# Optimization experiments

Hardware: AMD Instinct MI355X
Metric: run time of the kernel (lower is better)

Reference implementation:

```python
import jax, jax.numpy as jnp
import numpy as np

N_NODES = 50000

def setup_inputs() -> dict:
    key = jax.random.key(0)
    k1, k2, k3, k4, k5, k6, k7 = jax.random.split(key, 7)
    d_in, d_hid, d_out = 128, 512, 128
    n_edges = 600000
    x = jax.random.normal(k1, (N_NODES, d_in), dtype=jnp.float32)
    edge_index = jax.random.randint(k2, (2, n_edges), 0, N_NODES, dtype=jnp.int64)
    edge_weight = jax.random.uniform(k3, (n_edges,), dtype=jnp.float32)
    # GCNConv params (PyG: weight [in, out], bias [out])
    W1 = jax.random.normal(k4, (d_in, d_hid), dtype=jnp.float32) / np.sqrt(d_in)
    b1 = jax.random.normal(k5, (d_hid,), dtype=jnp.float32) * 0.01
    W2 = jax.random.normal(k6, (d_hid, d_out), dtype=jnp.float32) / np.sqrt(d_hid)
    b2 = jax.random.normal(k7, (d_out,), dtype=jnp.float32) * 0.01
    return {"x": x, "edge_index": edge_index, "edge_weight": edge_weight,
            "W1": W1, "b1": b1, "W2": W2, "b2": b2}

def gcn_conv(x, src, dst, ew, W, b, n_nodes):
    # PyG GCNConv: add self-loops (weight 1), symmetric normalization
    idx = jnp.arange(n_nodes, dtype=src.dtype)
    src_f = jnp.concatenate([src, idx])
    dst_f = jnp.concatenate([dst, idx])
    ew_f = jnp.concatenate([ew, jnp.ones((n_nodes,), dtype=ew.dtype)])
    deg = jax.ops.segment_sum(ew_f, dst_f, num_segments=n_nodes)
    dinv = jnp.where(deg > 0, jax.lax.rsqrt(deg), 0.0)
    norm = dinv[src_f] * ew_f * dinv[dst_f]  # [E+N]
    xw = x @ W  # [N, d_hid]
    msg = xw[src_f] * norm[:, None]  # [E+N, d_hid]
    agg = jax.ops.segment_sum(msg, dst_f, num_segments=n_nodes)
    return agg + b

def reference(x, edge_index, edge_weight, W1, b1, W2, b2):
    src, dst = edge_index[0], edge_index[1]
    h = gcn_conv(x, src, dst, edge_weight, W1, b1, N_NODES)
    h = jax.nn.relu(h)
    out = jax.nn.relu(h @ W2 + b2)
    return out
```

## Files before the change

### kernel.cpp

```cpp
#include <hip/hip_runtime.h>
#include <math.h>


typedef __attribute__((ext_vector_type(8))) short short8v;
typedef __attribute__((ext_vector_type(4))) float floatx4;

__device__ __forceinline__ short f2bf(float f) {
    unsigned u = __builtin_bit_cast(unsigned, f);
    unsigned r = (u + 0x7FFFu + ((u >> 16) & 1u)) >> 16;
    return (short)r;
}
__device__ __forceinline__ float bf2f(short s) {
    return __builtin_bit_cast(float, ((unsigned)(unsigned short)s) << 16);
}


__global__ __launch_bounds__(256) void k_init(int* __restrict__ counts,
                                              float* __restrict__ deg, int n) {
    int i = blockIdx.x * 256 + threadIdx.x;
    if (i < n) { counts[i] = 0; deg[i] = 1.0f; }
}

__global__ __launch_bounds__(256) void k_hist(const int* __restrict__ dst,
                                              const float* __restrict__ ew,
                                              int* __restrict__ counts,
                                              float* __restrict__ deg, int E) {
    int e = blockIdx.x * 256 + threadIdx.x;
    if (e < E) {
        int d = dst[e];
        atomicAdd(&counts[d], 1);
        atomicAdd(&deg[d], ew[e]);
    }
}

__global__ __launch_bounds__(256) void k_scanA(const int* __restrict__ counts,
                                               int* __restrict__ offsets,
                                               int* __restrict__ blockSum,
                                               float* __restrict__ deg, int n) {
    __shared__ int sdata[256];
    const int tid = threadIdx.x;
    const int i = blockIdx.x * 256 + tid;
    int c = (i < n) ? counts[i] : 0;
    sdata[tid] = c;
    __syncthreads();
#pragma unroll
    for (int off = 1; off < 256; off <<= 1) {
        int t = (tid >= off) ? sdata[tid - off] : 0;
        __syncthreads();
        sdata[tid] += t;
        __syncthreads();
    }
    if (i < n) offsets[i] = sdata[tid] - c;
    if (tid == 255) blockSum[blockIdx.x] = sdata[255];
    if (i < n) {
        float d = deg[i];
        deg[i] = (d > 0.f) ? rsqrtf(d) : 0.f;
    }
}

__global__ __launch_bounds__(256) void k_scanB(int* __restrict__ blockSum, int nb) {
    __shared__ int sdata[256];
    const int tid = threadIdx.x;
    int v = (tid < nb) ? blockSum[tid] : 0;
    sdata[tid] = v;
    __syncthreads();
#pragma unroll
    for (int off = 1; off < 256; off <<= 1) {
        int t = (tid >= off) ? sdata[tid - off] : 0;
        __syncthreads();
        sdata[tid] += t;
        __syncthreads();
    }
    if (tid < nb) blockSum[tid] = sdata[tid] - v;
}

__global__ __launch_bounds__(256) void k_scanC(int* __restrict__ offsets,
                                               const int* __restrict__ blockSum,
                                               int* __restrict__ cursor, int n, int E) {
    const int i = blockIdx.x * 256 + threadIdx.x;
    if (i < n) {
        int o = offsets[i] + blockSum[blockIdx.x];
        offsets[i] = o;
        cursor[i] = o;
    }
    if (i == 0) offsets[n] = E;
}

__global__ __launch_bounds__(256) void k_scatter(const int* __restrict__ src,
                                                 const int* __restrict__ dst,
                                                 const float* __restrict__ ew,
                                                 const float* __restrict__ dinv,
                                                 int* __restrict__ cursor,
                                                 int2* __restrict__ sedge, int E) {
    int e = blockIdx.x * 256 + threadIdx.x;
    if (e >= E) return;
    int s = src[e];
    int d = dst[e];
    float coef = dinv[s] * ew[e] * dinv[d];
    int pos = atomicAdd(&cursor[d], 1);
    sedge[pos] = make_int2(s, __builtin_bit_cast(int, coef));
}

__global__ __launch_bounds__(256) void k_gather(const int* __restrict__ offsets,
                                                const int2* __restrict__ sedge,
                                                const float* __restrict__ dinv,
                                                const float* __restrict__ x,
                                                float* __restrict__ y, int n) {
    int wid = (blockIdx.x * 256 + threadIdx.x) >> 6;
    if (wid >= n) return;
    int lane = threadIdx.x & 63;
    int o0 = offsets[wid];
    int o1 = offsets[wid + 1];
    float di = dinv[wid];
    const float2* x2 = (const float2*)x;
    float2 xv = x2[(size_t)wid * 64 + lane];
    float2 acc;
    acc.x = di * di * xv.x;
    acc.y = di * di * xv.y;
    int j = o0;
    for (; j + 4 <= o1; j += 4) {
        int2 e0 = sedge[j], e1 = sedge[j + 1], e2 = sedge[j + 2], e3 = sedge[j + 3];
        float2 v0 = x2[(size_t)e0.x * 64 + lane];
        float2 v1 = x2[(size_t)e1.x * 64 + lane];
        float2 v2 = x2[(size_t)e2.x * 64 + lane];
        float2 v3 = x2[(size_t)e3.x * 64 + lane];
        float c0 = __builtin_bit_cast(float, e0.y);
        float c1 = __builtin_bit_cast(float, e1.y);
        float c2 = __builtin_bit_cast(float, e2.y);
        float c3 = __builtin_bit_cast(float, e3.y);
        acc.x = fmaf(c0, v0.x, acc.x); acc.y = fmaf(c0, v0.y, acc.y);
        acc.x = fmaf(c1, v1.x, acc.x); acc.y = fmaf(c1, v1.y, acc.y);
        acc.x = fmaf(c2, v2.x, acc.x); acc.y = fmaf(c2, v2.y, acc.y);
        acc.x = fmaf(c3, v3.x, acc.x); acc.y = fmaf(c3, v3.y, acc.y);
    }
    for (; j < o1; ++j) {
        int2 e = sedge[j];
        float2 v = x2[(size_t)e.x * 64 + lane];
        float c = __builtin_bit_cast(float, e.y);
        acc.x = fmaf(c, v.x, acc.x);
        acc.y = fmaf(c, v.y, acc.y);
    }
    ((float2*)y)[(size_t)wid * 64 + lane] = acc;
}

__global__ __launch_bounds__(256) void k_wprep(const float* __restrict__ W1,
                                               const float* __restrict__ W2,
                                               short* __restrict__ W1t,
                                               short* __restrict__ W2t) {
    int i = blockIdx.x * 256 + threadIdx.x;
    if (i < 65536) {
        int c = i >> 7, k = i & 127;
        W1t[i] = f2bf(W1[k * 512 + c]);
    } else if (i < 131072) {
        int j = i - 65536;
        int c = j >> 9, k = j & 511;
        W2t[j] = f2bf(W2[k * 128 + c]);
    }
}

__global__ __launch_bounds__(256) void k_mlp(const float* __restrict__ y,
                                             const short* __restrict__ W1t,
                                             const float* __restrict__ b1,
                                             const short* __restrict__ W2t,
                                             const float* __restrict__ b2,
                                             float* __restrict__ out, int n) {
    __shared__ __align__(16) short hlds[32 * 512];
    const int tid  = threadIdx.x;
    const int wave = tid >> 6;
    const int lane = tid & 63;
    const int l15  = lane & 15;
    const int lg   = lane >> 4;
    const int row0 = blockIdx.x * 32;

    const int cb1 = wave * 128;
    floatx4 acc[2][8];
#pragma unroll
    for (int m = 0; m < 2; ++m)
#pragma unroll
        for (int nn = 0; nn < 8; ++nn) acc[m][nn] = (floatx4)0.0f;

#pragma unroll
    for (int kk = 0; kk < 4; ++kk) {
        const int k0 = kk * 32 + lg * 8;
        short8v bf[8];
#pragma unroll
        for (int nn = 0; nn < 8; ++nn)
            bf[nn] = *(const short8v*)(W1t + (size_t)(cb1 + nn * 16 + l15) * 128 + k0);
#pragma unroll
        for (int m = 0; m < 2; ++m) {
            const float* ap = y + (size_t)(row0 + m * 16 + l15) * 128 + k0;
            float4 f0 = *(const float4*)ap;
            float4 f1 = *(const float4*)(ap + 4);
            float fv[8] = {f0.x, f0.y, f0.z, f0.w, f1.x, f1.y, f1.z, f1.w};
            short8v ahi, alo;
#pragma unroll
            for (int i = 0; i < 8; ++i) {
                short h = f2bf(fv[i]);
                ahi[i] = h;
                alo[i] = f2bf(fv[i] - bf2f(h));
            }
#pragma unroll
            for (int nn = 0; nn < 8; ++nn)
                acc[m][nn] = __builtin_amdgcn_mfma_f32_16x16x32_bf16(ahi, bf[nn], acc[m][nn], 0, 0, 0);
#pragma unroll
            for (int nn = 0; nn < 8; ++nn)
                acc[m][nn] = __builtin_amdgcn_mfma_f32_16x16x32_bf16(alo, bf[nn], acc[m][nn], 0, 0, 0);
        }
    }

#pragma unroll
    for (int m = 0; m < 2; ++m)
#pragma unroll
        for (int nn = 0; nn < 8; ++nn) {
            const int c = cb1 + nn * 16 + l15;
            const float bb = b1[c];
#pragma unroll
            for (int i = 0; i < 4; ++i) {
                const int r = m * 16 + lg * 4 + i;
                float v = acc[m][nn][i] + bb;
                v = v > 0.f ? v : 0.f;
                hlds[r * 512 + (c ^ ((r & 7) << 3))] = f2bf(v);
            }
        }
    __syncthreads();

    const int cb2 = wave * 32;
    floatx4 acc2[2][2];
#pragma unroll
    for (int m = 0; m < 2; ++m)
#pragma unroll
        for (int nn = 0; nn < 2; ++nn) acc2[m][nn] = (floatx4)0.0f;

#pragma unroll
    for (int kk = 0; kk < 16; ++kk) {
        const int k0 = kk * 32 + lg * 8;
        short8v bf2[2];
#pragma unroll
        for (int nn = 0; nn < 2; ++nn)
            bf2[nn] = *(const short8v*)(W2t + (size_t)(cb2 + nn * 16 + l15) * 512 + k0);
#pragma unroll
        for (int m = 0; m < 2; ++m) {
            const int r = m * 16 + l15;
            short8v a = *(const short8v*)&hlds[r * 512 + (k0 ^ ((r & 7) << 3))];
#pragma unroll
            for (int nn = 0; nn < 2; ++nn)
                acc2[m][nn] = __builtin_amdgcn_mfma_f32_16x16x32_bf16(a, bf2[nn], acc2[m][nn], 0, 0, 0);
        }
    }

#pragma unroll
    for (int m = 0; m < 2; ++m)
#pragma unroll
        for (int nn = 0; nn < 2; ++nn) {
            const int c = cb2 + nn * 16 + l15;
            const float bb = b2[c];
#pragma unroll
            for (int i = 0; i < 4; ++i) {
                const int rg = row0 + m * 16 + lg * 4 + i;
                if (rg < n) {
                    float v = acc2[m][nn][i] + bb;
                    out[(size_t)rg * 128 + c] = v > 0.f ? v : 0.f;
                }
            }
        }
}

extern "C" void kernel_launch(void* const* d_in, const int* in_sizes, int n_in,
                              void* d_out, int out_size, void* d_ws, size_t ws_size,
                              hipStream_t stream) {
    const float* x  = (const float*)d_in[0];
    const int*   ei = (const int*)d_in[1];
    const float* ew = (const float*)d_in[2];
    const float* W1 = (const float*)d_in[3];
    const float* b1 = (const float*)d_in[4];
    const float* W2 = (const float*)d_in[5];
    const float* b2 = (const float*)d_in[6];
    float* out = (float*)d_out;

    const int N = in_sizes[0] / 128;
    const int E = in_sizes[2];
    const int* src = ei;
    const int* dst = ei + E;
    const int NB = (N + 255) / 256;

    float* y        = (float*)d_ws;
    float* deg      = y + (size_t)N * 128;
    int*   counts   = (int*)(deg + N);
    int*   offsets  = counts + N;
    int*   cursor   = offsets + N + 1;
    int*   blockSum = cursor + N;
    int2*  sedge    = (int2*)((((uintptr_t)(blockSum + 256)) + 15) & ~(uintptr_t)15);
    short* W1t      = (short*)(sedge + E);
    short* W2t      = W1t + 65536;

    int nb;
    k_wprep<<<512, 256, 0, stream>>>(W1, W2, W1t, W2t);
    nb = (N + 255) / 256;
    k_init<<<nb, 256, 0, stream>>>(counts, deg, N);
    nb = (E + 255) / 256;
    k_hist<<<nb, 256, 0, stream>>>(dst, ew, counts, deg, E);
    k_scanA<<<NB, 256, 0, stream>>>(counts, offsets, blockSum, deg, N);
    k_scanB<<<1, 256, 0, stream>>>(blockSum, NB);
    k_scanC<<<NB, 256, 0, stream>>>(offsets, blockSum, cursor, N, E);
    nb = (E + 255) / 256;
    k_scatter<<<nb, 256, 0, stream>>>(src, dst, ew, deg, cursor, sedge, E);
    nb = (N * 64 + 255) / 256;
    k_gather<<<nb, 256, 0, stream>>>(offsets, sedge, deg, x, y, N);
    nb = (N + 31) / 32;
    k_mlp<<<nb, 256, 0, stream>>>(y, W1t, b1, W2t, b2, out, N);
}
```

Before: 303.9 us.

## Fuse neighbor gather into MLP kernel via swizzled LDS, merge init with weight prep

The gather stage now runs inside the MLP kernel. Each block aggregates its 32 node rows into LDS as bf16 hi/lo pairs with an XOR swizzle, which removes the N×128 fp32 intermediate written to and read back from global memory. The separate cursor array is dropped: scatter advances offsets in place, and gather recovers each start as end minus count. The init and weight-prep kernels are merged to save a launch, but each MLP block now does gather work with only 4 waves of 8 rows, so there is less latency hiding for the random gathers.

```diff
diff --git a/kernel.cpp b/kernel.cpp
--- a/kernel.cpp
+++ b/kernel.cpp
@@ -14,11 +14,22 @@
     return __builtin_bit_cast(float, ((unsigned)(unsigned short)s) << 16);
 }
 
-
-__global__ __launch_bounds__(256) void k_init(int* __restrict__ counts,
-                                              float* __restrict__ deg, int n) {
+__global__ __launch_bounds__(256) void k_initprep(int* __restrict__ counts,
+                                                  float* __restrict__ deg, int n,
+                                                  const float* __restrict__ W1,
+                                                  const float* __restrict__ W2,
+                                                  short* __restrict__ W1t,
+                                                  short* __restrict__ W2t) {
     int i = blockIdx.x * 256 + threadIdx.x;
     if (i < n) { counts[i] = 0; deg[i] = 1.0f; }
+    if (i < 65536) {
+        int c = i >> 7, k = i & 127;
+        W1t[i] = f2bf(W1[k * 512 + c]);
+    } else if (i < 131072) {
+        int j = i - 65536;
+        int c = j >> 9, k = j & 511;
+        W2t[j] = f2bf(W2[k * 128 + c]);
+    }
 }
 
 __global__ __launch_bounds__(256) void k_hist(const int* __restrict__ dst,
@@ -75,95 +86,38 @@
 }
 
 __global__ __launch_bounds__(256) void k_scanC(int* __restrict__ offsets,
-                                               const int* __restrict__ blockSum,
-                                               int* __restrict__ cursor, int n, int E) {
+                                               const int* __restrict__ blockSum, int n) {
     const int i = blockIdx.x * 256 + threadIdx.x;
-    if (i < n) {
-        int o = offsets[i] + blockSum[blockIdx.x];
-        offsets[i] = o;
-        cursor[i] = o;
-    }
-    if (i == 0) offsets[n] = E;
+    if (i < n) offsets[i] += blockSum[blockIdx.x];
 }
 
 __global__ __launch_bounds__(256) void k_scatter(const int* __restrict__ src,
                                                  const int* __restrict__ dst,
                                                  const float* __restrict__ ew,
                                                  const float* __restrict__ dinv,
-                                                 int* __restrict__ cursor,
+                                                 int* __restrict__ offsets,
                                                  int2* __restrict__ sedge, int E) {
     int e = blockIdx.x * 256 + threadIdx.x;
     if (e >= E) return;
     int s = src[e];
     int d = dst[e];
     float coef = dinv[s] * ew[e] * dinv[d];
-    int pos = atomicAdd(&cursor[d], 1);
+    int pos = atomicAdd(&offsets[d], 1);
     sedge[pos] = make_int2(s, __builtin_bit_cast(int, coef));
 }
 
-__global__ __launch_bounds__(256) void k_gather(const int* __restrict__ offsets,
-                                                const int2* __restrict__ sedge,
-                                                const float* __restrict__ dinv,
-                                                const float* __restrict__ x,
-                                                float* __restrict__ y, int n) {
-    int wid = (blockIdx.x * 256 + threadIdx.x) >> 6;
-    if (wid >= n) return;
-    int lane = threadIdx.x & 63;
-    int o0 = offsets[wid];
-    int o1 = offsets[wid + 1];
-    float di = dinv[wid];
-    const float2* x2 = (const float2*)x;
-    float2 xv = x2[(size_t)wid * 64 + lane];
-    float2 acc;
-    acc.x = di * di * xv.x;
-    acc.y = di * di * xv.y;
-    int j = o0;
-    for (; j + 4 <= o1; j += 4) {
-        int2 e0 = sedge[j], e1 = sedge[j + 1], e2 = sedge[j + 2], e3 = sedge[j + 3];
-        float2 v0 = x2[(size_t)e0.x * 64 + lane];
-        float2 v1 = x2[(size_t)e1.x * 64 + lane];
-        float2 v2 = x2[(size_t)e2.x * 64 + lane];
-        float2 v3 = x2[(size_t)e3.x * 64 + lane];
-        float c0 = __builtin_bit_cast(float, e0.y);
-        float c1 = __builtin_bit_cast(float, e1.y);
-        float c2 = __builtin_bit_cast(float, e2.y);
-        float c3 = __builtin_bit_cast(float, e3.y);
-        acc.x = fmaf(c0, v0.x, acc.x); acc.y = fmaf(c0, v0.y, acc.y);
-        acc.x = fmaf(c1, v1.x, acc.x); acc.y = fmaf(c1, v1.y, acc.y);
-        acc.x = fmaf(c2, v2.x, acc.x); acc.y = fmaf(c2, v2.y, acc.y);
-        acc.x = fmaf(c3, v3.x, acc.x); acc.y = fmaf(c3, v3.y, acc.y);
-    }
-    for (; j < o1; ++j) {
-        int2 e = sedge[j];
-        float2 v = x2[(size_t)e.x * 64 + lane];
-        float c = __builtin_bit_cast(float, e.y);
-        acc.x = fmaf(c, v.x, acc.x);
-        acc.y = fmaf(c, v.y, acc.y);
-    }
-    ((float2*)y)[(size_t)wid * 64 + lane] = acc;
-}
-
-__global__ __launch_bounds__(256) void k_wprep(const float* __restrict__ W1,
-                                               const float* __restrict__ W2,
-                                               short* __restrict__ W1t,
-                                               short* __restrict__ W2t) {
-    int i = blockIdx.x * 256 + threadIdx.x;
-    if (i < 65536) {
-        int c = i >> 7, k = i & 127;
-        W1t[i] = f2bf(W1[k * 512 + c]);
-    } else if (i < 131072) {
-        int j = i - 65536;
-        int c = j >> 9, k = j & 511;
-        W2t[j] = f2bf(W2[k * 128 + c]);
-    }
-}
-
-__global__ __launch_bounds__(256) void k_mlp(const float* __restrict__ y,
-                                             const short* __restrict__ W1t,
-                                             const float* __restrict__ b1,
-                                             const short* __restrict__ W2t,
-                                             const float* __restrict__ b2,
-                                             float* __restrict__ out, int n) {
+__global__ __launch_bounds__(256) void k_gmlp(const int* __restrict__ offsets,
+                                              const int* __restrict__ counts,
+                                              const int2* __restrict__ sedge,
+                                              const float* __restrict__ dinv,
+                                              const float* __restrict__ x,
+                                              const short* __restrict__ W1t,
+                                              const float* __restrict__ b1,
+                                              const short* __restrict__ W2t,
+                                              const float* __restrict__ b2,
+                                              float* __restrict__ out, int n) {
+    __shared__ __align__(16) short yhi[32 * 128];
+    __shared__ __align__(16) short ylo[32 * 128];
     __shared__ __align__(16) short hlds[32 * 512];
     const int tid  = threadIdx.x;
     const int wave = tid >> 6;
@@ -171,6 +125,52 @@
     const int l15  = lane & 15;
     const int lg   = lane >> 4;
     const int row0 = blockIdx.x * 32;
+    const float2* x2 = (const float2*)x;
+
+    for (int i = 0; i < 8; ++i) {
+        const int r = wave * 8 + i;
+        const int node = row0 + r;
+        float2 acc = make_float2(0.f, 0.f);
+        if (node < n) {
+            int o1 = offsets[node];
+            int o0 = o1 - counts[node];
+            float di = dinv[node];
+            float2 xv = x2[(size_t)node * 64 + lane];
+            acc.x = di * di * xv.x;
+            acc.y = di * di * xv.y;
+            int j = o0;
+            for (; j + 4 <= o1; j += 4) {
+                int2 e0 = sedge[j], e1 = sedge[j + 1], e2 = sedge[j + 2], e3 = sedge[j + 3];
+                float2 v0 = x2[(size_t)e0.x * 64 + lane];
+                float2 v1 = x2[(size_t)e1.x * 64 + lane];
+                float2 v2 = x2[(size_t)e2.x * 64 + lane];
+                float2 v3 = x2[(size_t)e3.x * 64 + lane];
+                float c0 = __builtin_bit_cast(float, e0.y);
+                float c1 = __builtin_bit_cast(float, e1.y);
+                float c2 = __builtin_bit_cast(float, e2.y);
+                float c3 = __builtin_bit_cast(float, e3.y);
+                acc.x = fmaf(c0, v0.x, acc.x); acc.y = fmaf(c0, v0.y, acc.y);
+                acc.x = fmaf(c1, v1.x, acc.x); acc.y = fmaf(c1, v1.y, acc.y);
+                acc.x = fmaf(c2, v2.x, acc.x); acc.y = fmaf(c2, v2.y, acc.y);
+                acc.x = fmaf(c3, v3.x, acc.x); acc.y = fmaf(c3, v3.y, acc.y);
+            }
+            for (; j < o1; ++j) {
+                int2 e = sedge[j];
+                float2 v = x2[(size_t)e.x * 64 + lane];
+                float c = __builtin_bit_cast(float, e.y);
+                acc.x = fmaf(c, v.x, acc.x);
+                acc.y = fmaf(c, v.y, acc.y);
+            }
+        }
+        short hx = f2bf(acc.x);
+        short hy = f2bf(acc.y);
+        short lx = f2bf(acc.x - bf2f(hx));
+        short ly = f2bf(acc.y - bf2f(hy));
+        const int e = (2 * lane) ^ ((r & 7) << 3);
+        *(short2*)&yhi[r * 128 + e] = make_short2(hx, hy);
+        *(short2*)&ylo[r * 128 + e] = make_short2(lx, ly);
+    }
+    __syncthreads();
 
     const int cb1 = wave * 128;
     floatx4 acc[2][8];
@@ -188,17 +188,10 @@
             bf[nn] = *(const short8v*)(W1t + (size_t)(cb1 + nn * 16 + l15) * 128 + k0);
 #pragma unroll
         for (int m = 0; m < 2; ++m) {
-            const float* ap = y + (size_t)(row0 + m * 16 + l15) * 128 + k0;
-            float4 f0 = *(const float4*)ap;
-            float4 f1 = *(const float4*)(ap + 4);
-            float fv[8] = {f0.x, f0.y, f0.z, f0.w, f1.x, f1.y, f1.z, f1.w};
-            short8v ahi, alo;
-#pragma unroll
-            for (int i = 0; i < 8; ++i) {
-                short h = f2bf(fv[i]);
-                ahi[i] = h;
-                alo[i] = f2bf(fv[i] - bf2f(h));
-            }
+            const int r = m * 16 + l15;
+            const int ke = k0 ^ ((r & 7) << 3);
+            short8v ahi = *(const short8v*)&yhi[r * 128 + ke];
+            short8v alo = *(const short8v*)&ylo[r * 128 + ke];
 #pragma unroll
             for (int nn = 0; nn < 8; ++nn)
                 acc[m][nn] = __builtin_amdgcn_mfma_f32_16x16x32_bf16(ahi, bf[nn], acc[m][nn], 0, 0, 0);
@@ -283,29 +276,24 @@
     const int* dst = ei + E;
     const int NB = (N + 255) / 256;
 
-    float* y        = (float*)d_ws;
-    float* deg      = y + (size_t)N * 128;
+    float* deg      = (float*)d_ws;
     int*   counts   = (int*)(deg + N);
     int*   offsets  = counts + N;
-    int*   cursor   = offsets + N + 1;
-    int*   blockSum = cursor + N;
+    int*   blockSum = offsets + N;
     int2*  sedge    = (int2*)((((uintptr_t)(blockSum + 256)) + 15) & ~(uintptr_t)15);
     short* W1t      = (short*)(sedge + E);
     short* W2t      = W1t + 65536;
 
     int nb;
-    k_wprep<<<512, 256, 0, stream>>>(W1, W2, W1t, W2t);
-    nb = (N + 255) / 256;
-    k_init<<<nb, 256, 0, stream>>>(counts, deg, N);
+    k_initprep<<<512, 256, 0, stream>>>(counts, deg, N, W1, W2, W1t, W2t);
     nb = (E + 255) / 256;
     k_hist<<<nb, 256, 0, stream>>>(dst, ew, counts, deg, E);
     k_scanA<<<NB, 256, 0, stream>>>(counts, offsets, blockSum, deg, N);
     k_scanB<<<1, 256, 0, stream>>>(blockSum, NB);
-    k_scanC<<<NB, 256, 0, stream>>>(offsets, blockSum, cursor, N, E);
+    k_scanC<<<NB, 256, 0, stream>>>(offsets, blockSum, N);
     nb = (E + 255) / 256;
-    k_scatter<<<nb, 256, 0, stream>>>(src, dst, ew, deg, cursor, sedge, E);
-    nb = (N * 64 + 255) / 256;
-    k_gather<<<nb, 256, 0, stream>>>(offsets, sedge, deg, x, y, N);
+    k_scatter<<<nb, 256, 0, stream>>>(src, dst, ew, deg, offsets, sedge, E);
     nb = (N + 31) / 32;
-    k_mlp<<<nb, 256, 0, stream>>>(y, W1t, b1, W2t, b2, out, N);
-}
+    k_gmlp<<<nb, 256, 0, stream>>>(offsets, counts, sedge, deg, x,
+                                   W1t, b1, W2t, b2, out, N);
+}
```

Result: slower. 316.5 us (+4.1%).
